# Kernel tuning notes

Measured on AMD Instinct MI355X. Metric: run time of the kernel, lower is better.

The kernel has to match this reference:

```python
import jax, jax.numpy as jnp
import numpy as np
from jax import lax

C, H, W = 256, 512, 512


def setup_inputs() -> dict:
    key = jax.random.key(0)
    x = jax.random.normal(key, (C, H, W), dtype=jnp.float32)
    return {"x": x}


def reference(x):
    # Original torch code mutates x in-place: top pooling first (reverse
    # cummax along H, i.e. max over rows below), then left pooling on the
    # ALREADY top-pooled tensor (reverse cummax along W). `top` and `left`
    # alias the same storage, so out = t + t = 2 * t.
    t = lax.cummax(x, axis=1, reverse=True)   # top pool: propagate maxima upward
    t = lax.cummax(t, axis=2, reverse=True)   # left pool: propagate maxima leftward
    return t + t
```

## Files before the change

### kernel.cpp

```cpp
#include <hip/hip_runtime.h>
#include <math.h>

constexpr int C     = 256;
constexpr int H     = 512;
constexpr int W     = 512;
constexpr int RPW   = 4;
constexpr int BATCH = 8 * RPW;
constexpr int NB    = H / BATCH;

typedef float v4f __attribute__((ext_vector_type(4)));

__device__ __forceinline__ v4f vmax4(v4f a, v4f b) {
    v4f r;
    r.x = fmaxf(a.x, b.x); r.y = fmaxf(a.y, b.y);
    r.z = fmaxf(a.z, b.z); r.w = fmaxf(a.w, b.w);
    return r;
}

__global__ __launch_bounds__(512)
void tlc_kernel(const float* __restrict__ x, float* __restrict__ out) {
    const int tid  = threadIdx.x;
    const int g    = tid >> 6;
    const int lane = tid & 63;
    const int c    = blockIdx.x;
    const int col  = lane * 8;

    __shared__ v4f ltotA[2][8][64], ltotB[2][8][64];
    __shared__ v4f gcolA[2][64],    gcolB[2][64];

    const float* __restrict__ xc = x   + (size_t)c * H * W;
    float*       __restrict__ oc = out + (size_t)c * H * W;

    const int s1  = min(lane + 1, 63),  s2  = min(lane + 2, 63);
    const int s4  = min(lane + 4, 63),  s8  = min(lane + 8, 63);
    const int s16 = min(lane + 16, 63), s32 = min(lane + 32, 63);

    if (g == 0) {
        const v4f ninf = (v4f){-INFINITY, -INFINITY, -INFINITY, -INFINITY};
        gcolA[0][lane] = ninf;
        gcolB[0][lane] = ninf;
    }

    v4f b0A[RPW], b0B[RPW], b1A[RPW], b1B[RPW], b2A[RPW], b2B[RPW];

#define LOADB(bufA, bufB, t) {                                               \
    const float* p0 = xc + (size_t)(H - BATCH * ((t) + 1) + RPW * g) * W + col; \
    _Pragma("unroll")                                                        \
    for (int r = 0; r < RPW; ++r) {                                          \
        bufA[r] = __builtin_nontemporal_load((const v4f*)(p0 + (size_t)r * W));     \
        bufB[r] = __builtin_nontemporal_load((const v4f*)(p0 + (size_t)r * W + 4)); \
    } }

#define STEPC(bufA, bufB, t) {                                               \
    const int rb = H - BATCH * ((t) + 1) + RPW * g;                          \
    const int pb = (t) & 1;                                                  \
    _Pragma("unroll")                                                        \
    for (int r = 0; r < RPW; ++r) {                                          \
        const v4f a = bufA[r], b = bufB[r];                                  \
        const float t7 = b.w;                                                \
        const float t6 = fmaxf(b.z, t7);                                     \
        const float t5 = fmaxf(b.y, t6);                                     \
        const float t4 = fmaxf(b.x, t5);                                     \
        const float t3 = fmaxf(a.w, t4);                                     \
        const float t2 = fmaxf(a.z, t3);                                     \
        const float t1 = fmaxf(a.y, t2);                                     \
        const float t0 = fmaxf(a.x, t1);                                     \
        float e = __shfl(t0, s1);                                            \
        e = (lane == 63) ? -INFINITY : e;                                    \
        e = fmaxf(e, __shfl(e, s1));  e = fmaxf(e, __shfl(e, s2));           \
        e = fmaxf(e, __shfl(e, s4));  e = fmaxf(e, __shfl(e, s8));           \
        e = fmaxf(e, __shfl(e, s16)); e = fmaxf(e, __shfl(e, s32));          \
        bufA[r] = (v4f){fmaxf(t0, e), fmaxf(t1, e), fmaxf(t2, e), fmaxf(t3, e)}; \
        bufB[r] = (v4f){fmaxf(t4, e), fmaxf(t5, e), fmaxf(t6, e), fmaxf(t7, e)}; \
    }                                                                        \
    _Pragma("unroll")                                                        \
    for (int r = RPW - 2; r >= 0; --r) {                                     \
        bufA[r] = vmax4(bufA[r], bufA[r + 1]);                               \
        bufB[r] = vmax4(bufB[r], bufB[r + 1]);                               \
    }                                                                        \
    ltotA[pb][g][lane] = bufA[0];                                            \
    ltotB[pb][g][lane] = bufB[0];                                            \
    __syncthreads();                                                         \
    v4f mA = gcolA[pb][lane];                                                \
    v4f mB = gcolB[pb][lane];                                                \
    for (int gg = g + 1; gg < 8; ++gg) {                                     \
        mA = vmax4(mA, ltotA[pb][gg][lane]);                                 \
        mB = vmax4(mB, ltotB[pb][gg][lane]);                                 \
    }                                                                        \
    if (g == 0) {                                                            \
        gcolA[pb ^ 1][lane] = vmax4(bufA[0], mA);                            \
        gcolB[pb ^ 1][lane] = vmax4(bufB[0], mB);                            \
    }                                                                        \
    _Pragma("unroll")                                                        \
    for (int r = 0; r < RPW; ++r) {                                          \
        v4f oA = vmax4(bufA[r], mA) * 2.0f;                                  \
        v4f oB = vmax4(bufB[r], mB) * 2.0f;                                  \
        float* q = oc + (size_t)(rb + r) * W + col;                          \
        __builtin_nontemporal_store(oA, (v4f*)q);                            \
        __builtin_nontemporal_store(oB, (v4f*)(q + 4));                      \
    } }

    LOADB(b0A, b0B, 0)
    LOADB(b1A, b1B, 1)

    LOADB(b2A, b2B,  2)  STEPC(b0A, b0B,  0)
    LOADB(b0A, b0B,  3)  STEPC(b1A, b1B,  1)
    LOADB(b1A, b1B,  4)  STEPC(b2A, b2B,  2)
    LOADB(b2A, b2B,  5)  STEPC(b0A, b0B,  3)
    LOADB(b0A, b0B,  6)  STEPC(b1A, b1B,  4)
    LOADB(b1A, b1B,  7)  STEPC(b2A, b2B,  5)
    LOADB(b2A, b2B,  8)  STEPC(b0A, b0B,  6)
    LOADB(b0A, b0B,  9)  STEPC(b1A, b1B,  7)
    LOADB(b1A, b1B, 10)  STEPC(b2A, b2B,  8)
    LOADB(b2A, b2B, 11)  STEPC(b0A, b0B,  9)
    LOADB(b0A, b0B, 12)  STEPC(b1A, b1B, 10)
    LOADB(b1A, b1B, 13)  STEPC(b2A, b2B, 11)
    LOADB(b2A, b2B, 14)  STEPC(b0A, b0B, 12)
    LOADB(b0A, b0B, 15)  STEPC(b1A, b1B, 13)
                         STEPC(b2A, b2B, 14)
                         STEPC(b0A, b0B, 15)

#undef LOADB
#undef STEPC
}

extern "C" void kernel_launch(void* const* d_in, const int* in_sizes, int n_in,
                              void* d_out, int out_size, void* d_ws, size_t ws_size,
                              hipStream_t stream) {
    const float* x   = (const float*)d_in[0];
    float*       out = (float*)d_out;
    tlc_kernel<<<dim3(C), dim3(512), 0, stream>>>(x, out);
}
```

Before: 109.5 us.

## Split each channel across two blocks with flag-based cross-block row handoff

Each channel's width is split into two halves handled by separate blocks, which doubles the grid to 2*C blocks for more parallelism. The right half writes per-row totals to a workspace and sets release flags. The left-half block spin-waits on those flags and folds the totals into its own leftward max. An init kernel clears the flags first. This adds a second launch, inter-block spin dependencies that could deadlock if the left blocks are scheduled before the right ones, and extra atomic traffic.

```diff
diff --git a/kernel.cpp b/kernel.cpp
--- a/kernel.cpp
+++ b/kernel.cpp
@@ -7,6 +7,7 @@
 constexpr int RPW   = 4;
 constexpr int BATCH = 8 * RPW;
 constexpr int NB    = H / BATCH;
+constexpr int HALF  = W / 2;
 
 typedef float v4f __attribute__((ext_vector_type(4)));
 
@@ -17,8 +18,135 @@
     return r;
 }
 
+__global__ void tlc_init(int* __restrict__ flg, int n) {
+    int i = blockIdx.x * blockDim.x + threadIdx.x;
+    if (i < n) flg[i] = 0;
+}
+
+__global__ __launch_bounds__(512, 4)
+void tlc_split(const float* __restrict__ x, float* __restrict__ out,
+               float* __restrict__ tot, int* __restrict__ flg) {
+    const int bb   = blockIdx.x;
+    const int side = bb >> 8;
+    const int c    = bb & 255;
+    const int tid  = threadIdx.x;
+    const int g    = tid >> 6;
+    const int lane = tid & 63;
+    const int col  = (side == 0 ? HALF : 0) + lane * 4;
+
+    __shared__ v4f ltot[2][8][64];
+    __shared__ v4f gcol[2][64];
+
+    const float* __restrict__ xc   = x   + (size_t)c * H * W;
+    float*       __restrict__ oc   = out + (size_t)c * H * W;
+    float*       __restrict__ totc = tot + (size_t)c * H;
+    int*         __restrict__ flgc = flg + (size_t)c * NB;
+
+    const int s1  = min(lane + 1, 63),  s2  = min(lane + 2, 63);
+    const int s4  = min(lane + 4, 63),  s8  = min(lane + 8, 63);
+    const int s16 = min(lane + 16, 63), s32 = min(lane + 32, 63);
+
+    if (g == 0) {
+        const v4f ninf = (v4f){-INFINITY, -INFINITY, -INFINITY, -INFINITY};
+        gcol[0][lane] = ninf;
+    }
+
+    v4f b0[RPW], b1[RPW], b2[RPW];
+
+#define LOADB(buf, t) {                                                      \
+    const float* p0 = xc + (size_t)(H - BATCH * ((t) + 1) + RPW * g) * W + col; \
+    _Pragma("unroll")                                                        \
+    for (int r = 0; r < RPW; ++r)                                            \
+        buf[r] = __builtin_nontemporal_load((const v4f*)(p0 + (size_t)r * W)); \
+    }
+
+#define STEPC(buf, t) {                                                      \
+    const int rb = H - BATCH * ((t) + 1) + RPW * g;                          \
+    const int pb = (t) & 1;                                                  \
+                                \
+    _Pragma("unroll")                                                        \
+    for (int r = 0; r < RPW; ++r) {                                          \
+        const v4f a = buf[r];                                                \
+        const float u3 = a.w;                                                \
+        const float u2 = fmaxf(a.z, u3);                                     \
+        const float u1 = fmaxf(a.y, u2);                                     \
+        const float u0 = fmaxf(a.x, u1);                                     \
+        float e = __shfl(u0, s1);                                            \
+        e = (lane == 63) ? -INFINITY : e;                                    \
+        e = fmaxf(e, __shfl(e, s1));  e = fmaxf(e, __shfl(e, s2));           \
+        e = fmaxf(e, __shfl(e, s4));  e = fmaxf(e, __shfl(e, s8));           \
+        e = fmaxf(e, __shfl(e, s16)); e = fmaxf(e, __shfl(e, s32));          \
+        buf[r] = (v4f){fmaxf(u0, e), fmaxf(u1, e), fmaxf(u2, e), fmaxf(u3, e)}; \
+    }                                                                        \
+                                                   \
+    _Pragma("unroll")                                                        \
+    for (int r = RPW - 2; r >= 0; --r) buf[r] = vmax4(buf[r], buf[r + 1]);   \
+    ltot[pb][g][lane] = buf[0];                                              \
+    __syncthreads();                                                         \
+    v4f mA = gcol[pb][lane];                                                 \
+    for (int gg = g + 1; gg < 8; ++gg) mA = vmax4(mA, ltot[pb][gg][lane]);   \
+    if (g == 0) gcol[pb ^ 1][lane] = vmax4(buf[0], mA);                      \
+    if (side == 0) {                                                         \
+             \
+        _Pragma("unroll")                                                    \
+        for (int r = 0; r < RPW; ++r) {                                      \
+            const v4f m = vmax4(buf[r], mA);                                 \
+            float* q = oc + (size_t)(rb + r) * W + col;                      \
+            __builtin_nontemporal_store(m * 2.0f, (v4f*)q);                  \
+            if (lane == 0)                                                   \
+                __hip_atomic_store(&totc[rb + r], m.x, __ATOMIC_RELAXED,     \
+                                   __HIP_MEMORY_SCOPE_AGENT);                \
+        }                                                                    \
+        __syncthreads();     \
+        if (tid == 0)                                                        \
+            __hip_atomic_store(&flgc[(t)], 1, __ATOMIC_RELEASE,              \
+                               __HIP_MEMORY_SCOPE_AGENT);                    \
+    } else {                                                                 \
+           \
+        if (tid == 0) {                                                      \
+            while (__hip_atomic_load(&flgc[(t)], __ATOMIC_ACQUIRE,           \
+                                     __HIP_MEMORY_SCOPE_AGENT) == 0)         \
+                __builtin_amdgcn_s_sleep(1);                                 \
+        }                                                                    \
+        __syncthreads();                                                     \
+        _Pragma("unroll")                                                    \
+        for (int r = 0; r < RPW; ++r) {                                      \
+            const float rt = __hip_atomic_load(&totc[rb + r],                \
+                                               __ATOMIC_RELAXED,             \
+                                               __HIP_MEMORY_SCOPE_AGENT);    \
+            v4f m = vmax4(buf[r], mA);                                       \
+            m = vmax4(m, (v4f){rt, rt, rt, rt});                             \
+            float* q = oc + (size_t)(rb + r) * W + col;                      \
+            __builtin_nontemporal_store(m * 2.0f, (v4f*)q);                  \
+        }                                                                    \
+    } }
+
+    LOADB(b0, 0)
+    LOADB(b1, 1)
+
+    LOADB(b2,  2)  STEPC(b0,  0)
+    LOADB(b0,  3)  STEPC(b1,  1)
+    LOADB(b1,  4)  STEPC(b2,  2)
+    LOADB(b2,  5)  STEPC(b0,  3)
+    LOADB(b0,  6)  STEPC(b1,  4)
+    LOADB(b1,  7)  STEPC(b2,  5)
+    LOADB(b2,  8)  STEPC(b0,  6)
+    LOADB(b0,  9)  STEPC(b1,  7)
+    LOADB(b1, 10)  STEPC(b2,  8)
+    LOADB(b2, 11)  STEPC(b0,  9)
+    LOADB(b0, 12)  STEPC(b1, 10)
+    LOADB(b1, 13)  STEPC(b2, 11)
+    LOADB(b2, 14)  STEPC(b0, 12)
+    LOADB(b0, 15)  STEPC(b1, 13)
+                   STEPC(b2, 14)
+                   STEPC(b0, 15)
+
+#undef LOADB
+#undef STEPC
+}
+
 __global__ __launch_bounds__(512)
-void tlc_kernel(const float* __restrict__ x, float* __restrict__ out) {
+void tlc_fallback(const float* __restrict__ x, float* __restrict__ out) {
     const int tid  = threadIdx.x;
     const int g    = tid >> 6;
     const int lane = tid & 63;
@@ -57,21 +185,21 @@
     _Pragma("unroll")                                                        \
     for (int r = 0; r < RPW; ++r) {                                          \
         const v4f a = bufA[r], b = bufB[r];                                  \
-        const float t7 = b.w;                                                \
-        const float t6 = fmaxf(b.z, t7);                                     \
-        const float t5 = fmaxf(b.y, t6);                                     \
-        const float t4 = fmaxf(b.x, t5);                                     \
-        const float t3 = fmaxf(a.w, t4);                                     \
-        const float t2 = fmaxf(a.z, t3);                                     \
-        const float t1 = fmaxf(a.y, t2);                                     \
-        const float t0 = fmaxf(a.x, t1);                                     \
-        float e = __shfl(t0, s1);                                            \
+        const float u7 = b.w;                                                \
+        const float u6 = fmaxf(b.z, u7);                                     \
+        const float u5 = fmaxf(b.y, u6);                                     \
+        const float u4 = fmaxf(b.x, u5);                                     \
+        const float u3 = fmaxf(a.w, u4);                                     \
+        const float u2 = fmaxf(a.z, u3);                                     \
+        const float u1 = fmaxf(a.y, u2);                                     \
+        const float u0 = fmaxf(a.x, u1);                                     \
+        float e = __shfl(u0, s1);                                            \
         e = (lane == 63) ? -INFINITY : e;                                    \
         e = fmaxf(e, __shfl(e, s1));  e = fmaxf(e, __shfl(e, s2));           \
         e = fmaxf(e, __shfl(e, s4));  e = fmaxf(e, __shfl(e, s8));           \
         e = fmaxf(e, __shfl(e, s16)); e = fmaxf(e, __shfl(e, s32));          \
-        bufA[r] = (v4f){fmaxf(t0, e), fmaxf(t1, e), fmaxf(t2, e), fmaxf(t3, e)}; \
-        bufB[r] = (v4f){fmaxf(t4, e), fmaxf(t5, e), fmaxf(t6, e), fmaxf(t7, e)}; \
+        bufA[r] = (v4f){fmaxf(u0, e), fmaxf(u1, e), fmaxf(u2, e), fmaxf(u3, e)}; \
+        bufB[r] = (v4f){fmaxf(u4, e), fmaxf(u5, e), fmaxf(u6, e), fmaxf(u7, e)}; \
     }                                                                        \
     _Pragma("unroll")                                                        \
     for (int r = RPW - 2; r >= 0; --r) {                                     \
@@ -129,5 +257,17 @@
                               hipStream_t stream) {
     const float* x   = (const float*)d_in[0];
     float*       out = (float*)d_out;
-    tlc_kernel<<<dim3(C), dim3(512), 0, stream>>>(x, out);
-}
+
+    const size_t needTot = (size_t)C * H * sizeof(float);
+    const size_t needFlg = (size_t)C * NB * sizeof(int);
+
+    if (ws_size >= needTot + needFlg) {
+        float* tot = (float*)d_ws;
+        int*   flg = (int*)((char*)d_ws + needTot);
+        const int nflags = C * NB;
+        tlc_init<<<dim3((nflags + 255) / 256), dim3(256), 0, stream>>>(flg, nflags);
+        tlc_split<<<dim3(2 * C), dim3(512), 0, stream>>>(x, out, tot, flg);
+    } else {
+        tlc_fallback<<<dim3(C), dim3(512), 0, stream>>>(x, out);
+    }
+}
```

Result: slower. 324.2 us (+196.0%).
